# Kernel tuning notes

Hardware: AMD Instinct MI355X
Metric: run time of the kernel (lower is better)

The kernel has to match this reference:

```python
import jax, jax.numpy as jnp
import numpy as np

N_DEPTH = 4
N_STACKS = 2
INPUT_SIZE = 1024
HIDDEN_SIZE = 4096
HU = HIDDEN_SIZE // (N_DEPTH * N_STACKS)  # unit_hidden_size = 512
BATCH = 4096


def setup_inputs() -> dict:
    key = jax.random.key(0)
    ks = jax.random.split(key, 8)
    inp = {
        "input": jax.random.normal(ks[0], (BATCH, INPUT_SIZE), dtype=jnp.float32),
        "state": jax.random.normal(ks[1], (2, N_STACKS, BATCH, HIDDEN_SIZE), dtype=jnp.float32),
        # LSTMCell params; residualStack=True -> every cell input dim = INPUT_SIZE
        "W_ih": jax.random.normal(ks[2], (N_DEPTH, N_STACKS, 4 * HU, INPUT_SIZE), dtype=jnp.float32) * 0.05,
        "W_hh": jax.random.normal(ks[3], (N_DEPTH, N_STACKS, 4 * HU, HU), dtype=jnp.float32) * 0.05,
        "b_ih": jax.random.normal(ks[4], (N_DEPTH, N_STACKS, 4 * HU), dtype=jnp.float32) * 0.05,
        "b_hh": jax.random.normal(ks[5], (N_DEPTH, N_STACKS, 4 * HU), dtype=jnp.float32) * 0.05,
        # stacks_proj: Linear(HU, INPUT_SIZE)
        "proj_W": jax.random.normal(ks[6], (INPUT_SIZE, HU), dtype=jnp.float32) * 0.05,
        "proj_b": jax.random.normal(ks[7], (INPUT_SIZE,), dtype=jnp.float32) * 0.05,
    }
    return inp


def _lstm_cell(x, hx, cx, w_ih, w_hh, b_ih, b_hh):
    # gates: [B, 4*HU], PyTorch LSTMCell gate order: i, f, g, o
    gates = x @ w_ih.T + b_ih + hx @ w_hh.T + b_hh
    i_g, f_g, g_g, o_g = jnp.split(gates, 4, axis=-1)
    i_g = jax.nn.sigmoid(i_g)
    f_g = jax.nn.sigmoid(f_g)
    g_g = jnp.tanh(g_g)
    o_g = jax.nn.sigmoid(o_g)
    c_out = f_g * cx + i_g * g_g
    h_out = o_g * jnp.tanh(c_out)
    return h_out, c_out


def reference(input, state, W_ih, W_hh, b_ih, b_hh, proj_W, proj_b):
    # residual=True, residualStack=True
    h_depth, c_depth = [], []
    for i in range(N_DEPTH):
        s, e = i * HU, (i + 1) * HU
        hs, cs = [], []
        dec_input = input
        h_out = None
        for j in range(N_STACKS):
            if j > 0:
                # residualStack: dec_input = dec_input + stacks_proj(h_out)
                dec_input = dec_input + h_out @ proj_W.T + proj_b
            hx = state[0, j, :, s:e]
            cx = state[1, j, :, s:e]
            h_out, c_out = _lstm_cell(dec_input, hx, cx,
                                      W_ih[i, j], W_hh[i, j], b_ih[i, j], b_hh[i, j])
            hs.append(h_out + hx)  # residual=True
            cs.append(c_out)
        h_depth.append(jnp.stack(hs, 0))  # [nStacks, B, HU]
        c_depth.append(jnp.stack(cs, 0))
    # hidden dim is laid out by depth slice: newState[..., i*HU:(i+1)*HU]
    newH = jnp.concatenate(h_depth, axis=-1)  # [nStacks, B, hidden_size]
    newC = jnp.concatenate(c_depth, axis=-1)
    newState = jnp.stack([newH, newC], axis=0)  # [2, nStacks, B, hidden_size]
    ho = newState[0, -1]  # [B, hidden_size]
    return ho, newState
```

## Files before the change

kernel.cpp:

```cpp
#include <hip/hip_runtime.h>
#include <cstdint>
#include <cstddef>

#define B_   4096
#define ISZ  1024
#define SW   4096
#define OHW  2048
#define HU_  512
#define NG   2048

typedef float f32x4 __attribute__((ext_vector_type(4)));
typedef short bf16x8 __attribute__((ext_vector_type(8)));

__device__ __forceinline__ short f2bf(float x) {
    union { float f; unsigned u; } v; v.f = x;
    unsigned r = v.u + 0x7fffu + ((v.u >> 16) & 1u);
    return (short)(r >> 16);
}
__device__ __forceinline__ float sigm(float x)   { return 1.f / (1.f + __expf(-x)); }
__device__ __forceinline__ float tanh_f(float x) { return 2.f / (1.f + __expf(-2.f * x)) - 1.f; }

__device__ __forceinline__ void async16(const void* g, void* l) {
    __builtin_amdgcn_global_load_lds((__attribute__((address_space(1))) void*)g,
                                     (__attribute__((address_space(3))) void*)l,
                                     16, 0, 0);
}

#define VM_BAR(N) asm volatile("s_waitcnt vmcnt(" #N ")\n\ts_barrier" ::: "memory")

__global__ __launch_bounds__(256) void cvt_kernel(const float* __restrict__ src,
                                                  short* __restrict__ dst, long n) {
    long i = ((long)blockIdx.x * 256 + threadIdx.x) * 8;
    if (i >= n) return;
    float4 a = *(const float4*)(src + i);
    float4 b = *(const float4*)(src + i + 4);
    bf16x8 o;
    o[0] = f2bf(a.x); o[1] = f2bf(a.y); o[2] = f2bf(a.z); o[3] = f2bf(a.w);
    o[4] = f2bf(b.x); o[5] = f2bf(b.y); o[6] = f2bf(b.z); o[7] = f2bf(b.w);
    *(bf16x8*)(dst + i) = o;
}

__global__ __launch_bounds__(256) void cvt_h_kernel(const float* __restrict__ src,
                                                    short* __restrict__ dst) {
    long i = ((long)blockIdx.x * 256 + threadIdx.x) * 8;
    long row = i >> 11;
    long c   = i & 2047;
    const float* s = src + row * SW + c;
    float4 a = *(const float4*)(s);
    float4 b = *(const float4*)(s + 4);
    bf16x8 o;
    o[0] = f2bf(a.x); o[1] = f2bf(a.y); o[2] = f2bf(a.z); o[3] = f2bf(a.w);
    o[4] = f2bf(b.x); o[5] = f2bf(b.y); o[6] = f2bf(b.z); o[7] = f2bf(b.w);
    *(bf16x8*)(dst + i) = o;
}

#define MMA_BLK(BB, AR0, N0)                                                      \
  do {                                                                            \
    __builtin_amdgcn_s_setprio(1);                                                \
    _Pragma("unroll")                                                             \
    for (int mtl = 0; mtl < 4; ++mtl) {                                           \
      _Pragma("unroll")                                                           \
      for (int nn = 0; nn < 2; ++nn) {                                            \
        _Pragma("unroll")                                                         \
        for (int ks = 0; ks < 2; ++ks) {                                          \
          acc[(AR0) + mtl][(N0) + nn] = __builtin_amdgcn_mfma_f32_16x16x32_bf16(  \
              aR[mtl][ks], BB[nn][ks], acc[(AR0) + mtl][(N0) + nn], 0, 0, 0);     \
        }                                                                         \
      }                                                                           \
    }                                                                             \
    __builtin_amdgcn_s_setprio(0);                                                \
  } while (0)

#define GROW(rb) (((((rb) >> 4) & 3) << 9) + h0 + ((((rb) >> 6)) << 4) + ((rb) & 15))

__global__ __launch_bounds__(512, 2) void gates2_kernel(
    const short* __restrict__ A1, long a1_dstride,
    const short* __restrict__ Hb,
    const short* __restrict__ Wihb, const short* __restrict__ Whhb,
    const float* __restrict__ b_ih, const float* __restrict__ b_hh,
    const float* __restrict__ state,
    float* __restrict__ out_ho, float* __restrict__ out_state,
    short* __restrict__ h0b,
    int j)
{
    extern __shared__ short lds[];

    const int tid  = threadIdx.x;
    const int wave = tid >> 6;
    const int lane = tid & 63;
    const int wm   = wave >> 2;
    const int wn   = wave & 3;
    const int ln16 = lane & 15;
    const int q    = (lane >> 4) & 3;

    const int id  = blockIdx.x;
    const int swz = (id & 7) * 64 + (id >> 3);
    const int M0  = (swz & 15) * 256;
    const int h0  = ((swz >> 4) & 7) * 64;
    const int d   = swz >> 7;
    const int s   = d * HU_;

    const short* A1d = A1 + (size_t)d * a1_dstride;
    const short* A2  = Hb + (size_t)j * B_ * OHW + s;
    const short* W1  = Wihb + (size_t)(d * 2 + j) * NG * ISZ;
    const short* W2  = Whhb + (size_t)(d * 2 + j) * NG * HU_;
    const float* bi_ = b_ih + (size_t)(d * 2 + j) * NG;
    const float* bh_ = b_hh + (size_t)(d * 2 + j) * NG;

    const int srow = tid >> 3;
    const int scol = (((tid & 7) ^ ((tid >> 3) & 7)) << 3);

    const short* As = A1d;
    const short* Bs = W1;
    unsigned aoff0 = (unsigned)((M0 +   0 + srow) * ISZ + scol);
    unsigned aoff1 = (unsigned)((M0 +  64 + srow) * ISZ + scol);
    unsigned aoff2 = (unsigned)((M0 + 128 + srow) * ISZ + scol);
    unsigned aoff3 = (unsigned)((M0 + 192 + srow) * ISZ + scol);
    unsigned boff0 = (unsigned)(GROW(      srow) * ISZ + scol);
    unsigned boff1 = (unsigned)(GROW( 64 + srow) * ISZ + scol);
    unsigned boff2 = (unsigned)(GROW(128 + srow) * ISZ + scol);
    unsigned boff3 = (unsigned)(GROW(192 + srow) * ISZ + scol);

    const int swz0 = ((q    ) ^ (ln16 & 7)) << 4;
    const int swz1 = ((q + 4) ^ (ln16 & 7)) << 4;
    const char* ldsb = (const char*)lds;

    f32x4 acc[8][4];
#pragma unroll
    for (int i = 0; i < 8; ++i)
#pragma unroll
        for (int n = 0; n < 4; ++n) acc[i][n] = (f32x4){0.f, 0.f, 0.f, 0.f};

    bf16x8 aR[4][2];
    bf16x8 b01[2][2];
    bf16x8 b23[2][2];

    auto stA = [&](unsigned off, int it, int nbuf, int kofs) {
        async16(As + off + kofs, lds + nbuf * 32768 + (it * 64 + wave * 8) * 64);
    };
    auto stB = [&](unsigned off, int it, int nbuf, int kofs) {
        async16(Bs + off + kofs, lds + nbuf * 32768 + 16384 + (it * 64 + wave * 8) * 64);
    };
    auto rdA = [&](int buf, int hi) {
#pragma unroll
        for (int mtl = 0; mtl < 4; ++mtl) {
            const int row = wm * 128 + hi * 64 + mtl * 16 + ln16;
            aR[mtl][0] = *(const bf16x8*)(ldsb + buf * 65536 + row * 128 + swz0);
            aR[mtl][1] = *(const bf16x8*)(ldsb + buf * 65536 + row * 128 + swz1);
        }
    };
    auto rdB = [&](bf16x8 (&bb)[2][2], int buf, int nt0) {
#pragma unroll
        for (int nn = 0; nn < 2; ++nn) {
            const int row = wn * 64 + (nt0 + nn) * 16 + ln16;
            bb[nn][0] = *(const bf16x8*)(ldsb + buf * 65536 + 32768 + row * 128 + swz0);
            bb[nn][1] = *(const bf16x8*)(ldsb + buf * 65536 + 32768 + row * 128 + swz1);
        }
    };

    stB(boff0, 0, 0, 0); stB(boff1, 1, 0, 0); stB(boff2, 2, 0, 0); stB(boff3, 3, 0, 0);
    stA(aoff0, 0, 0, 0); stA(aoff2, 2, 0, 0); stA(aoff1, 1, 0, 0); stA(aoff3, 3, 0, 0);
    VM_BAR(0);

    auto do_tile = [&](int t, int kofs) {
        const int buf = t & 1, nbuf = buf ^ 1;
        stB(boff0, 0, nbuf, kofs); stB(boff1, 1, nbuf, kofs);
        rdA(buf, 0); rdB(b01, buf, 0);
        MMA_BLK(b01, 0, 0);
        stB(boff2, 2, nbuf, kofs); stB(boff3, 3, nbuf, kofs);
        rdB(b23, buf, 2);
        MMA_BLK(b23, 0, 2);
        VM_BAR(4);
        stA(aoff0, 0, nbuf, kofs); stA(aoff2, 2, nbuf, kofs);
        rdA(buf, 1);
        MMA_BLK(b23, 4, 2);
        stA(aoff1, 1, nbuf, kofs); stA(aoff3, 3, nbuf, kofs);
        MMA_BLK(b01, 4, 0);
        VM_BAR(2);
    };

    for (int t = 0; t < 15; ++t) do_tile(t, (t + 1) * 64);

    As = A2; Bs = W2;
    aoff0 = (unsigned)((M0 +   0 + srow) * OHW + scol);
    aoff1 = (unsigned)((M0 +  64 + srow) * OHW + scol);
    aoff2 = (unsigned)((M0 + 128 + srow) * OHW + scol);
    aoff3 = (unsigned)((M0 + 192 + srow) * OHW + scol);
    boff0 = (unsigned)(GROW(      srow) * HU_ + scol);
    boff1 = (unsigned)(GROW( 64 + srow) * HU_ + scol);
    boff2 = (unsigned)(GROW(128 + srow) * HU_ + scol);
    boff3 = (unsigned)(GROW(192 + srow) * HU_ + scol);

    for (int t = 15; t < 23; ++t) do_tile(t, (t - 15) * 64);

    {
        rdA(1, 0); rdB(b01, 1, 0);
        MMA_BLK(b01, 0, 0);
        rdB(b23, 1, 2);
        MMA_BLK(b23, 0, 2);
        VM_BAR(0);
        rdA(1, 1);
        MMA_BLK(b23, 4, 2);
        MMA_BLK(b01, 4, 0);
    }

    const int h   = h0 + wn * 16 + ln16;
    const int col = s + h;
    const float b_i = bi_[h]          + bh_[h];
    const float b_f = bi_[512 + h]    + bh_[512 + h];
    const float b_g = bi_[1024 + h]   + bh_[1024 + h];
    const float b_o = bi_[1536 + h]   + bh_[1536 + h];
#pragma unroll
    for (int mt = 0; mt < 8; ++mt) {
#pragma unroll
        for (int r = 0; r < 4; ++r) {
            const int m = M0 + wm * 128 + mt * 16 + q * 4 + r;
            const float hx = state[((size_t)(j)     * B_ + m) * SW + col];
            const float cx = state[((size_t)(2 + j) * B_ + m) * SW + col];
            const float gi = sigm(acc[mt][0][r] + b_i);
            const float gf = sigm(acc[mt][1][r] + b_f);
            const float gg = tanh_f(acc[mt][2][r] + b_g);
            const float go = sigm(acc[mt][3][r] + b_o);
            const float c_out = gf * cx + gi * gg;
            const float h_out = go * tanh_f(c_out);
            out_state[((size_t)(j)     * B_ + m) * OHW + col] = h_out + hx;
            out_state[((size_t)(2 + j) * B_ + m) * OHW + col] = c_out;
            if (j == 1) out_ho[(size_t)m * OHW + col] = h_out + hx;
            else        h0b[((size_t)d * B_ + m) * HU_ + h] = f2bf(h_out);
        }
    }
}

__global__ __launch_bounds__(256, 2) void proj3_kernel(
    const short* __restrict__ h0b, const short* __restrict__ PWb,
    const float* __restrict__ input, const float* __restrict__ proj_b,
    short* __restrict__ dec1b)
{
    extern __shared__ short lds[];

    const int t    = threadIdx.x;
    const int wave = t >> 6, lane = t & 63;
    const int ln16 = lane & 15, q = lane >> 4;

    const int id  = blockIdx.x;
    const int swz = (id & 7) * 128 + (id >> 3);
    const int M0  = (swz & 31) * 128;
    const int N0  = ((swz >> 5) & 7) * 128;
    const int d   = swz >> 8;

    const short* A = h0b + (size_t)d * B_ * HU_;
    const short* Bm = PWb;

    const int srow = t >> 3;
    const int scol = (((t & 7) ^ ((t >> 3) & 7)) << 3);

    unsigned aoff[4], boff[4];
#pragma unroll
    for (int it = 0; it < 4; ++it) {
        aoff[it] = (unsigned)((M0 + it * 32 + srow) * HU_ + scol);
        boff[it] = (unsigned)((N0 + it * 32 + srow) * HU_ + scol);
    }

    f32x4 acc[2][8];
#pragma unroll
    for (int mt = 0; mt < 2; mt++)
#pragma unroll
        for (int nt = 0; nt < 8; nt++) acc[mt][nt] = (f32x4){0.f, 0.f, 0.f, 0.f};

    auto stage = [&](int nbuf, int k0) {
#pragma unroll
        for (int it = 0; it < 4; it++)
            async16(A + aoff[it] + k0, lds + nbuf * 16384 + (it * 32 + wave * 8) * 64);
#pragma unroll
        for (int it = 0; it < 4; it++)
            async16(Bm + boff[it] + k0, lds + nbuf * 16384 + 8192 + (it * 32 + wave * 8) * 64);
    };
    auto compute = [&](int buf) {
        const short* sA = lds + buf * 16384;
        const short* sB = lds + buf * 16384 + 8192;
#pragma unroll
        for (int ks = 0; ks < 2; ks++) {
            const int kb = ks * 4 + q;
            bf16x8 a[2], b[8];
#pragma unroll
            for (int mt = 0; mt < 2; mt++) {
                const int m = wave * 32 + mt * 16 + ln16;
                a[mt] = *(const bf16x8*)&sA[m * 64 + ((kb ^ (m & 7)) << 3)];
            }
#pragma unroll
            for (int nt = 0; nt < 8; nt++) {
                const int n = nt * 16 + ln16;
                b[nt] = *(const bf16x8*)&sB[n * 64 + ((kb ^ (n & 7)) << 3)];
            }
#pragma unroll
            for (int mt = 0; mt < 2; mt++)
#pragma unroll
                for (int nt = 0; nt < 8; nt++)
                    acc[mt][nt] = __builtin_amdgcn_mfma_f32_16x16x32_bf16(a[mt], b[nt], acc[mt][nt], 0, 0, 0);
        }
    };

    stage(0, 0);
    VM_BAR(0);

    for (int tt = 0; tt < 7; ++tt) {
        const int buf = tt & 1;
        stage(buf ^ 1, (tt + 1) * 64);
        compute(buf);
        VM_BAR(0);
    }
    compute(1);

#pragma unroll
    for (int mt = 0; mt < 2; mt++) {
#pragma unroll
        for (int nt = 0; nt < 8; nt++) {
            const int n = N0 + nt * 16 + ln16;
            const float pb = proj_b[n];
#pragma unroll
            for (int r = 0; r < 4; r++) {
                const int m = M0 + wave * 32 + mt * 16 + q * 4 + r;
                const float y = acc[mt][nt][r] + input[(size_t)m * ISZ + n] + pb;
                dec1b[((size_t)d * B_ + m) * ISZ + n] = f2bf(y);
            }
        }
    }
}

extern "C" void kernel_launch(void* const* d_in, const int* in_sizes, int n_in,
                              void* d_out, int out_size, void* d_ws, size_t ws_size,
                              hipStream_t stream)
{
    const float* input  = (const float*)d_in[0];
    const float* state  = (const float*)d_in[1];
    const float* W_ih   = (const float*)d_in[2];
    const float* W_hh   = (const float*)d_in[3];
    const float* b_ih   = (const float*)d_in[4];
    const float* b_hh   = (const float*)d_in[5];
    const float* proj_W = (const float*)d_in[6];
    const float* proj_b = (const float*)d_in[7];

    float* out_ho    = (float*)d_out;
    float* out_state = out_ho + (size_t)B_ * OHW;

    short* ws    = (short*)d_ws;
    short* Wihb  = ws;
    short* Whhb  = Wihb + (size_t)8 * NG * ISZ;
    short* PWb   = Whhb + (size_t)8 * NG * HU_;
    short* Hb    = PWb  + (size_t)ISZ * HU_;
    short* h0b   = Hb   + (size_t)2 * B_ * OHW;
    short* dec1b = h0b  + (size_t)4 * B_ * HU_;
    short* Xb    = dec1b;

    static bool s_attr = false;
    if (!s_attr) {
        (void)hipFuncSetAttribute(reinterpret_cast<const void*>(gates2_kernel),
                                  hipFuncAttributeMaxDynamicSharedMemorySize, 131072);
        (void)hipFuncSetAttribute(reinterpret_cast<const void*>(proj3_kernel),
                                  hipFuncAttributeMaxDynamicSharedMemorySize, 65536);
        s_attr = true;
    }

    {
        long n;
        n = (long)8 * NG * ISZ;  cvt_kernel<<<dim3((unsigned)(n / 8 / 256)), 256, 0, stream>>>(W_ih,   Wihb, n);
        n = (long)8 * NG * HU_;  cvt_kernel<<<dim3((unsigned)(n / 8 / 256)), 256, 0, stream>>>(W_hh,   Whhb, n);
        n = (long)ISZ * HU_;     cvt_kernel<<<dim3((unsigned)(n / 8 / 256)), 256, 0, stream>>>(proj_W, PWb,  n);
        n = (long)B_ * ISZ;      cvt_kernel<<<dim3((unsigned)(n / 8 / 256)), 256, 0, stream>>>(input,  Xb,   n);
        n = (long)2 * B_ * OHW;  cvt_h_kernel<<<dim3((unsigned)(n / 8 / 256)), 256, 0, stream>>>(state, Hb);
    }

    gates2_kernel<<<dim3(512), dim3(512), 131072, stream>>>(Xb, 0L, Hb, Wihb, Whhb,
                                                            b_ih, b_hh, state,
                                                            out_ho, out_state, h0b, 0);
    proj3_kernel<<<dim3(1024), dim3(256), 65536, stream>>>(h0b, PWb, input, proj_b, dec1b);
    gates2_kernel<<<dim3(512), dim3(512), 131072, stream>>>(dec1b, (long)B_ * ISZ, Hb, Wihb, Whhb,
                                                            b_ih, b_hh, state,
                                                            out_ho, out_state, nullptr, 1);
}
```

Before: 723.6 us.

## Pre-pack activations into MFMA fragment layout and load A directly to registers

Activations (input, hidden state, projected dec input) are written in a packed 16x32 fragment layout by the conversion and projection kernels, so the gates kernel loads A operands straight from global memory into registers instead of staging them through LDS. Only the weight tiles are double-buffered in LDS, which halves shared memory per block to 64KB and simplifies the pipeline to one barrier per tile. The cost is uncached, per-wave global loads of A in the critical loop with less latency hiding. Launch bounds also drop the min-blocks hint.

Measured after the change: 883.3 us. 22.1% more time.

```diff
diff --git a/kernel.cpp b/kernel.cpp
--- a/kernel.cpp
+++ b/kernel.cpp
@@ -8,6 +8,11 @@
 #define OHW  2048
 #define HU_  512
 #define NG   2048
+
+#define PK_SUB   512
+#define PK_NKB1  32
+#define PK_NKB2  16
+#define PK_DSTR  (256 * 32 * 512)
 
 typedef float f32x4 __attribute__((ext_vector_type(4)));
 typedef short bf16x8 __attribute__((ext_vector_type(8)));
@@ -40,21 +45,41 @@
     *(bf16x8*)(dst + i) = o;
 }
 
-__global__ __launch_bounds__(256) void cvt_h_kernel(const float* __restrict__ src,
-                                                    short* __restrict__ dst) {
+__global__ __launch_bounds__(256) void cvt_pack_kernel(const float* __restrict__ src,
+                                                       short* __restrict__ dst) {
     long i = ((long)blockIdx.x * 256 + threadIdx.x) * 8;
-    long row = i >> 11;
-    long c   = i & 2047;
+    const int m = (int)(i >> 10), c = (int)(i & 1023);
+    float4 a = *(const float4*)(src + i);
+    float4 b = *(const float4*)(src + i + 4);
+    bf16x8 o;
+    o[0] = f2bf(a.x); o[1] = f2bf(a.y); o[2] = f2bf(a.z); o[3] = f2bf(a.w);
+    o[4] = f2bf(b.x); o[5] = f2bf(b.y); o[6] = f2bf(b.z); o[7] = f2bf(b.w);
+    size_t off = ((size_t)(m >> 4) * PK_NKB1 + (c >> 5)) * PK_SUB
+               + ((((c >> 3) & 3) * 16) + (m & 15)) * 8;
+    *(bf16x8*)(dst + off) = o;
+}
+
+__global__ __launch_bounds__(256) void cvt_h_pack_kernel(const float* __restrict__ src,
+                                                         short* __restrict__ dst) {
+    long i = ((long)blockIdx.x * 256 + threadIdx.x) * 8;
+    const long row = i >> 11;
+    const int  c   = (int)(i & 2047);
+    const int  j   = (int)(row >> 12);
+    const int  m   = (int)(row & 4095);
+    const int  d   = c >> 9;
+    const int  k   = c & 511;
     const float* s = src + row * SW + c;
     float4 a = *(const float4*)(s);
     float4 b = *(const float4*)(s + 4);
     bf16x8 o;
     o[0] = f2bf(a.x); o[1] = f2bf(a.y); o[2] = f2bf(a.z); o[3] = f2bf(a.w);
     o[4] = f2bf(b.x); o[5] = f2bf(b.y); o[6] = f2bf(b.z); o[7] = f2bf(b.w);
-    *(bf16x8*)(dst + i) = o;
-}
-
-#define MMA_BLK(BB, AR0, N0)                                                      \
+    size_t off = ((size_t)(j * 4 + d) * 4096 + (size_t)(m >> 4) * PK_NKB2 + (k >> 5)) * PK_SUB
+               + ((((k >> 3) & 3) * 16) + (m & 15)) * 8;
+    *(bf16x8*)(dst + off) = o;
+}
+
+#define MMA_BLK(BB, AA, AR0, N0)                                                  \
   do {                                                                            \
     __builtin_amdgcn_s_setprio(1);                                                \
     _Pragma("unroll")                                                             \
@@ -64,7 +89,7 @@
         _Pragma("unroll")                                                         \
         for (int ks = 0; ks < 2; ++ks) {                                          \
           acc[(AR0) + mtl][(N0) + nn] = __builtin_amdgcn_mfma_f32_16x16x32_bf16(  \
-              aR[mtl][ks], BB[nn][ks], acc[(AR0) + mtl][(N0) + nn], 0, 0, 0);     \
+              AA[mtl][ks], BB[nn][ks], acc[(AR0) + mtl][(N0) + nn], 0, 0, 0);     \
         }                                                                         \
       }                                                                           \
     }                                                                             \
@@ -73,9 +98,9 @@
 
 #define GROW(rb) (((((rb) >> 4) & 3) << 9) + h0 + ((((rb) >> 6)) << 4) + ((rb) & 15))
 
-__global__ __launch_bounds__(512, 2) void gates2_kernel(
-    const short* __restrict__ A1, long a1_dstride,
-    const short* __restrict__ Hb,
+__global__ __launch_bounds__(512) void gates3_kernel(
+    const short* __restrict__ Apk, long a_dstride,
+    const short* __restrict__ Hpk,
     const short* __restrict__ Wihb, const short* __restrict__ Whhb,
     const float* __restrict__ b_ih, const float* __restrict__ b_hh,
     const float* __restrict__ state,
@@ -100,8 +125,8 @@
     const int d   = swz >> 7;
     const int s   = d * HU_;
 
-    const short* A1d = A1 + (size_t)d * a1_dstride;
-    const short* A2  = Hb + (size_t)j * B_ * OHW + s;
+    const short* A1p = Apk + (size_t)d * a_dstride;
+    const short* A2p = Hpk + (size_t)(j * 4 + d) * (4096 * PK_SUB);
     const short* W1  = Wihb + (size_t)(d * 2 + j) * NG * ISZ;
     const short* W2  = Whhb + (size_t)(d * 2 + j) * NG * HU_;
     const float* bi_ = b_ih + (size_t)(d * 2 + j) * NG;
@@ -110,99 +135,81 @@
     const int srow = tid >> 3;
     const int scol = (((tid & 7) ^ ((tid >> 3) & 7)) << 3);
 
-    const short* As = A1d;
-    const short* Bs = W1;
-    unsigned aoff0 = (unsigned)((M0 +   0 + srow) * ISZ + scol);
-    unsigned aoff1 = (unsigned)((M0 +  64 + srow) * ISZ + scol);
-    unsigned aoff2 = (unsigned)((M0 + 128 + srow) * ISZ + scol);
-    unsigned aoff3 = (unsigned)((M0 + 192 + srow) * ISZ + scol);
-    unsigned boff0 = (unsigned)(GROW(      srow) * ISZ + scol);
-    unsigned boff1 = (unsigned)(GROW( 64 + srow) * ISZ + scol);
-    unsigned boff2 = (unsigned)(GROW(128 + srow) * ISZ + scol);
-    unsigned boff3 = (unsigned)(GROW(192 + srow) * ISZ + scol);
+    unsigned b1off[4], b2off[4];
+#pragma unroll
+    for (int it = 0; it < 4; ++it) {
+        const int gr = GROW(it * 64 + srow);
+        b1off[it] = (unsigned)(gr * ISZ + scol);
+        b2off[it] = (unsigned)(gr * HU_ + scol);
+    }
 
     const int swz0 = ((q    ) ^ (ln16 & 7)) << 4;
     const int swz1 = ((q + 4) ^ (ln16 & 7)) << 4;
     const char* ldsb = (const char*)lds;
 
+    const int row16 = (M0 >> 4) + wm * 8;
+    const int l8    = lane * 8;
+
     f32x4 acc[8][4];
 #pragma unroll
     for (int i = 0; i < 8; ++i)
 #pragma unroll
         for (int n = 0; n < 4; ++n) acc[i][n] = (f32x4){0.f, 0.f, 0.f, 0.f};
 
-    bf16x8 aR[4][2];
-    bf16x8 b01[2][2];
-    bf16x8 b23[2][2];
-
-    auto stA = [&](unsigned off, int it, int nbuf, int kofs) {
-        async16(As + off + kofs, lds + nbuf * 32768 + (it * 64 + wave * 8) * 64);
-    };
-    auto stB = [&](unsigned off, int it, int nbuf, int kofs) {
-        async16(Bs + off + kofs, lds + nbuf * 32768 + 16384 + (it * 64 + wave * 8) * 64);
-    };
-    auto rdA = [&](int buf, int hi) {
+    bf16x8 aLo[4][2], aHi[4][2];
+    bf16x8 b01[2][2], b23[2][2];
+
+    auto stB = [&](const short* bsrc, const unsigned* bo, int nbuf, int kofs) {
+#pragma unroll
+        for (int it = 0; it < 4; ++it)
+            async16(bsrc + bo[it] + kofs, lds + nbuf * 16384 + (it * 64 + wave * 8) * 64);
+    };
+    auto ldA = [&](const short* apk, int nkb, int kblk) {
 #pragma unroll
         for (int mtl = 0; mtl < 4; ++mtl) {
-            const int row = wm * 128 + hi * 64 + mtl * 16 + ln16;
-            aR[mtl][0] = *(const bf16x8*)(ldsb + buf * 65536 + row * 128 + swz0);
-            aR[mtl][1] = *(const bf16x8*)(ldsb + buf * 65536 + row * 128 + swz1);
+            const short* p = apk + ((size_t)(row16 + mtl) * nkb + kblk) * PK_SUB + l8;
+            aLo[mtl][0] = *(const bf16x8*)(p);
+            aLo[mtl][1] = *(const bf16x8*)(p + PK_SUB);
+        }
+#pragma unroll
+        for (int mtl = 0; mtl < 4; ++mtl) {
+            const short* p = apk + ((size_t)(row16 + 4 + mtl) * nkb + kblk) * PK_SUB + l8;
+            aHi[mtl][0] = *(const bf16x8*)(p);
+            aHi[mtl][1] = *(const bf16x8*)(p + PK_SUB);
         }
     };
     auto rdB = [&](bf16x8 (&bb)[2][2], int buf, int nt0) {
 #pragma unroll
         for (int nn = 0; nn < 2; ++nn) {
             const int row = wn * 64 + (nt0 + nn) * 16 + ln16;
-            bb[nn][0] = *(const bf16x8*)(ldsb + buf * 65536 + 32768 + row * 128 + swz0);
-            bb[nn][1] = *(const bf16x8*)(ldsb + buf * 65536 + 32768 + row * 128 + swz1);
-        }
-    };
-
-    stB(boff0, 0, 0, 0); stB(boff1, 1, 0, 0); stB(boff2, 2, 0, 0); stB(boff3, 3, 0, 0);
-    stA(aoff0, 0, 0, 0); stA(aoff2, 2, 0, 0); stA(aoff1, 1, 0, 0); stA(aoff3, 3, 0, 0);
+            bb[nn][0] = *(const bf16x8*)(ldsb + buf * 32768 + row * 128 + swz0);
+            bb[nn][1] = *(const bf16x8*)(ldsb + buf * 32768 + row * 128 + swz1);
+        }
+    };
+
+    auto do_tile = [&](const short* apk, int nkb, int kblk, int buf,
+                       const short* bsrc, const unsigned* bo, int bkofs, bool doStage) {
+        ldA(apk, nkb, kblk);
+        asm volatile("" ::: "memory");
+        if (doStage) stB(bsrc, bo, buf ^ 1, bkofs);
+        rdB(b01, buf, 0);
+        MMA_BLK(b01, aLo, 0, 0);
+        rdB(b23, buf, 2);
+        MMA_BLK(b23, aLo, 0, 2);
+        MMA_BLK(b23, aHi, 4, 2);
+        MMA_BLK(b01, aHi, 4, 0);
+        VM_BAR(0);
+    };
+
+    stB(W1, b1off, 0, 0);
     VM_BAR(0);
 
-    auto do_tile = [&](int t, int kofs) {
-        const int buf = t & 1, nbuf = buf ^ 1;
-        stB(boff0, 0, nbuf, kofs); stB(boff1, 1, nbuf, kofs);
-        rdA(buf, 0); rdB(b01, buf, 0);
-        MMA_BLK(b01, 0, 0);
-        stB(boff2, 2, nbuf, kofs); stB(boff3, 3, nbuf, kofs);
-        rdB(b23, buf, 2);
-        MMA_BLK(b23, 0, 2);
-        VM_BAR(4);
-        stA(aoff0, 0, nbuf, kofs); stA(aoff2, 2, nbuf, kofs);
-        rdA(buf, 1);
-        MMA_BLK(b23, 4, 2);
-        stA(aoff1, 1, nbuf, kofs); stA(aoff3, 3, nbuf, kofs);
-        MMA_BLK(b01, 4, 0);
-        VM_BAR(2);
-    };
-
-    for (int t = 0; t < 15; ++t) do_tile(t, (t + 1) * 64);
-
-    As = A2; Bs = W2;
-    aoff0 = (unsigned)((M0 +   0 + srow) * OHW + scol);
-    aoff1 = (unsigned)((M0 +  64 + srow) * OHW + scol);
-    aoff2 = (unsigned)((M0 + 128 + srow) * OHW + scol);
-    aoff3 = (unsigned)((M0 + 192 + srow) * OHW + scol);
-    boff0 = (unsigned)(GROW(      srow) * HU_ + scol);
-    boff1 = (unsigned)(GROW( 64 + srow) * HU_ + scol);
-    boff2 = (unsigned)(GROW(128 + srow) * HU_ + scol);
-    boff3 = (unsigned)(GROW(192 + srow) * HU_ + scol);
-
-    for (int t = 15; t < 23; ++t) do_tile(t, (t - 15) * 64);
-
-    {
-        rdA(1, 0); rdB(b01, 1, 0);
-        MMA_BLK(b01, 0, 0);
-        rdB(b23, 1, 2);
-        MMA_BLK(b23, 0, 2);
-        VM_BAR(0);
-        rdA(1, 1);
-        MMA_BLK(b23, 4, 2);
-        MMA_BLK(b01, 4, 0);
-    }
+    for (int t = 0; t < 15; ++t)
+        do_tile(A1p, PK_NKB1, t * 2, t & 1, W1, b1off, (t + 1) * 64, true);
+    do_tile(A1p, PK_NKB1, 30, 1, W2, b2off, 0, true);
+    for (int t = 16; t < 23; ++t)
+        do_tile(A2p, PK_NKB2, (t - 16) * 2, t & 1, W2, b2off, (t - 15) * 64, true);
+    do_tile(A2p, PK_NKB2, 14, 1, W2, b2off, 0, false);
 
     const int h   = h0 + wn * 16 + ln16;
     const int col = s + h;
@@ -234,7 +241,7 @@
 __global__ __launch_bounds__(256, 2) void proj3_kernel(
     const short* __restrict__ h0b, const short* __restrict__ PWb,
     const float* __restrict__ input, const float* __restrict__ proj_b,
-    short* __restrict__ dec1b)
+    short* __restrict__ dec1pk)
 {
     extern __shared__ short lds[];
 
@@ -302,7 +309,6 @@
 
     stage(0, 0);
     VM_BAR(0);
-
     for (int tt = 0; tt < 7; ++tt) {
         const int buf = tt & 1;
         stage(buf ^ 1, (tt + 1) * 64);
@@ -311,17 +317,19 @@
     }
     compute(1);
 
+    const size_t dbase = (size_t)d * PK_DSTR;
 #pragma unroll
     for (int mt = 0; mt < 2; mt++) {
 #pragma unroll
         for (int nt = 0; nt < 8; nt++) {
             const int n = N0 + nt * 16 + ln16;
             const float pb = proj_b[n];
+            const size_t nPart = ((size_t)(n >> 5)) * PK_SUB + (((n >> 3) & 3) * 16) * 8 + (n & 7);
 #pragma unroll
             for (int r = 0; r < 4; r++) {
                 const int m = M0 + wave * 32 + mt * 16 + q * 4 + r;
                 const float y = acc[mt][nt][r] + input[(size_t)m * ISZ + n] + pb;
-                dec1b[((size_t)d * B_ + m) * ISZ + n] = f2bf(y);
+                dec1pk[dbase + ((size_t)(m >> 4) * PK_NKB1) * PK_SUB + nPart + (m & 15) * 8] = f2bf(y);
             }
         }
     }
@@ -343,19 +351,19 @@
     float* out_ho    = (float*)d_out;
     float* out_state = out_ho + (size_t)B_ * OHW;
 
-    short* ws    = (short*)d_ws;
-    short* Wihb  = ws;
-    short* Whhb  = Wihb + (size_t)8 * NG * ISZ;
-    short* PWb   = Whhb + (size_t)8 * NG * HU_;
-    short* Hb    = PWb  + (size_t)ISZ * HU_;
-    short* h0b   = Hb   + (size_t)2 * B_ * OHW;
-    short* dec1b = h0b  + (size_t)4 * B_ * HU_;
-    short* Xb    = dec1b;
+    short* ws     = (short*)d_ws;
+    short* Wihb   = ws;
+    short* Whhb   = Wihb + (size_t)8 * NG * ISZ;
+    short* PWb    = Whhb + (size_t)8 * NG * HU_;
+    short* Hpk    = PWb  + (size_t)ISZ * HU_;
+    short* h0b    = Hpk  + (size_t)2 * B_ * OHW;
+    short* dec1pk = h0b  + (size_t)4 * B_ * HU_;
+    short* Xpk    = dec1pk;
 
     static bool s_attr = false;
     if (!s_attr) {
-        (void)hipFuncSetAttribute(reinterpret_cast<const void*>(gates2_kernel),
-                                  hipFuncAttributeMaxDynamicSharedMemorySize, 131072);
+        (void)hipFuncSetAttribute(reinterpret_cast<const void*>(gates3_kernel),
+                                  hipFuncAttributeMaxDynamicSharedMemorySize, 65536);
         (void)hipFuncSetAttribute(reinterpret_cast<const void*>(proj3_kernel),
                                   hipFuncAttributeMaxDynamicSharedMemorySize, 65536);
         s_attr = true;
@@ -366,15 +374,15 @@
         n = (long)8 * NG * ISZ;  cvt_kernel<<<dim3((unsigned)(n / 8 / 256)), 256, 0, stream>>>(W_ih,   Wihb, n);
         n = (long)8 * NG * HU_;  cvt_kernel<<<dim3((unsigned)(n / 8 / 256)), 256, 0, stream>>>(W_hh,   Whhb, n);
         n = (long)ISZ * HU_;     cvt_kernel<<<dim3((unsigned)(n / 8 / 256)), 256, 0, stream>>>(proj_W, PWb,  n);
-        n = (long)B_ * ISZ;      cvt_kernel<<<dim3((unsigned)(n / 8 / 256)), 256, 0, stream>>>(input,  Xb,   n);
-        n = (long)2 * B_ * OHW;  cvt_h_kernel<<<dim3((unsigned)(n / 8 / 256)), 256, 0, stream>>>(state, Hb);
-    }
-
-    gates2_kernel<<<dim3(512), dim3(512), 131072, stream>>>(Xb, 0L, Hb, Wihb, Whhb,
-                                                            b_ih, b_hh, state,
-                                                            out_ho, out_state, h0b, 0);
-    proj3_kernel<<<dim3(1024), dim3(256), 65536, stream>>>(h0b, PWb, input, proj_b, dec1b);
-    gates2_kernel<<<dim3(512), dim3(512), 131072, stream>>>(dec1b, (long)B_ * ISZ, Hb, Wihb, Whhb,
-                                                            b_ih, b_hh, state,
-                                                            out_ho, out_state, nullptr, 1);
-}
+        n = (long)B_ * ISZ;      cvt_pack_kernel<<<dim3((unsigned)(n / 8 / 256)), 256, 0, stream>>>(input, Xpk);
+        n = (long)2 * B_ * OHW;  cvt_h_pack_kernel<<<dim3((unsigned)(n / 8 / 256)), 256, 0, stream>>>(state, Hpk);
+    }
+
+    gates3_kernel<<<dim3(512), dim3(512), 65536, stream>>>(Xpk, 0L, Hpk, Wihb, Whhb,
+                                                           b_ih, b_hh, state,
+                                                           out_ho, out_state, h0b, 0);
+    proj3_kernel<<<dim3(1024), dim3(256), 65536, stream>>>(h0b, PWb, input, proj_b, dec1pk);
+    gates3_kernel<<<dim3(512), dim3(512), 65536, stream>>>(dec1pk, (long)PK_DSTR, Hpk, Wihb, Whhb,
+                                                           b_ih, b_hh, state,
+                                                           out_ho, out_state, nullptr, 1);
+}
```
